# Kernel optimization log

Measured on AMD Instinct MI355X. Metric: run time of the kernel, lower is better.

## Reference

```python
import jax, jax.numpy as jnp
import numpy as np

ALPHA = 0.2          # LeakyReLU slope
THRESH = 0.6         # adjacency connection threshold
NEG_INF = -9e15      # masked-softmax fill used by the original


def setup_inputs() -> dict:
    key = jax.random.key(0)
    ks = jax.random.split(key, 5)
    B, N, F = 32, 512, 128
    h = jax.random.normal(ks[0], (B, N, F), dtype=jnp.float32)
    # torch nn.Linear weights: y = x @ W.T
    W = jax.random.normal(ks[1], (F, F), dtype=jnp.float32) * 0.1
    a = jax.random.normal(ks[2], (2 * F, 1), dtype=jnp.float32) * 0.1
    A0 = jax.random.normal(ks[3], (4 * N, N), dtype=jnp.float32) * 0.05
    A2 = jax.random.normal(ks[4], (N, 4 * N), dtype=jnp.float32) * 0.05
    return {"h": h, "W": W, "a": a, "A0": A0, "A2": A2}


def reference(h, W, a, A0, A2):
    F = W.shape[0]
    # Wh = W(h)                                  [B, N, F]
    Wh = jnp.einsum("bnf,gf->bng", h, W)
    # attention logits e = leakyrelu(Wh a1 + (Wh a2)^T)   [B, N, N]
    Wh1 = Wh @ a[:F]                              # [B, N, 1]
    Wh2 = Wh @ a[F:]                              # [B, N, 1]
    e = jax.nn.leaky_relu(Wh1 + jnp.swapaxes(Wh2, 1, 2), ALPHA)
    # learned adjacency MLP over last (node) dim: Linear -> Sigmoid -> Linear
    adj = e + jnp.einsum("bnk,mk->bnm", jax.nn.sigmoid(jnp.einsum("bnm,km->bnk", e, A0)), A2)
    # threshold + mask + softmax
    adj = jnp.where(adj > THRESH, adj, 0.0)
    att = jnp.where(adj > 0, e, NEG_INF)
    att = jax.nn.softmax(att, axis=2)
    # dropout is identity in eval mode
    h_prime = jnp.einsum("bnm,bmf->bnf", att, Wh)
    return jax.nn.elu(h_prime)                    # concat=True branch
```

## Files before the change

### kernel.cpp

```cpp
#include <hip/hip_runtime.h>

#define BB 32
#define NN 512
#define FF 128
#define K4 2048
#define ALPHA 0.2f
#define THRESH 0.6f
#define NEGINF -9e15f

typedef unsigned short u16;
typedef unsigned int u32;
typedef _Float16 f16;
typedef __attribute__((ext_vector_type(8))) _Float16 half8;
typedef __attribute__((ext_vector_type(4))) float f32x4;

union U16F { u16 u; f16 h; };
__device__ __forceinline__ u16 hbits(f16 h) { U16F x; x.h = h; return x.u; }
__device__ __forceinline__ float htof(u16 u) { U16F x; x.u = u; return (float)x.h; }
__device__ __forceinline__ void split2(float v, u16& hi, u16& lo) {
    f16 h = (f16)v;
    f16 l = (f16)(v - (float)h);
    hi = hbits(h);
    lo = hbits(l);
}
__device__ __forceinline__ float lrelu(float x) { return fmaxf(x, ALPHA * x); }

__device__ __forceinline__ void gload16(const void* g, void* l) {
    __builtin_amdgcn_global_load_lds(
        (__attribute__((address_space(1))) const unsigned int*)(unsigned long long)g,
        (__attribute__((address_space(3))) unsigned int*)(unsigned int)(unsigned long long)l,
        16, 0, 0);
}

__global__ void k_u(const float* __restrict__ W, const float* __restrict__ a,
                    float* __restrict__ u12) {
    int f = threadIdx.x;
    float s1 = 0.f, s2 = 0.f;
    for (int g = 0; g < FF; ++g) {
        float w = W[g * FF + f];
        s1 += w * a[g];
        s2 += w * a[FF + g];
    }
    u12[f] = s1;
    u12[FF + f] = s2;
}

__global__ void k_wh12(const float* __restrict__ h, const float* __restrict__ u12,
                       float* __restrict__ Wh12) {
    int row = blockIdx.x;
    int f = threadIdx.x;
    float hv = h[(size_t)row * FF + f];
    float p1 = hv * u12[f], p2 = hv * u12[FF + f];
#pragma unroll
    for (int o = 1; o < 64; o <<= 1) {
        p1 += __shfl_xor(p1, o, 64);
        p2 += __shfl_xor(p2, o, 64);
    }
    __shared__ float s1[2], s2[2];
    int w = f >> 6;
    if ((f & 63) == 0) { s1[w] = p1; s2[w] = p2; }
    __syncthreads();
    if (f == 0) {
        Wh12[row] = s1[0] + s1[1];
        Wh12[BB * NN + row] = s2[0] + s2[1];
    }
}

__global__ __launch_bounds__(256) void k_whT(const float* __restrict__ W,
                                             const float* __restrict__ h,
                                             u16* __restrict__ Thi, u16* __restrict__ Tlo) {
    const int bm = blockIdx.y * 64, bn = blockIdx.x * 64;
    __shared__ float As[32][68];
    __shared__ float Bs[32][68];
    int tid = threadIdx.x;
    int tx = tid & 15, ty = tid >> 4;
    float acc[4][4] = {{0.f}};
    int r = tid >> 3, q = tid & 7;
    const float* Ap = W + (size_t)(bm + r) * FF + q * 4;
    const float* Bp = h + (size_t)(bn + r) * FF + q * 4;
    for (int k0 = 0; k0 < FF; k0 += 32) {
        float4 a0 = *(const float4*)(Ap + k0);
        float4 a1 = *(const float4*)(Ap + k0 + 32 * FF);
        float4 b0 = *(const float4*)(Bp + k0);
        float4 b1 = *(const float4*)(Bp + k0 + 32 * FF);
        __syncthreads();
        As[q * 4 + 0][r] = a0.x; As[q * 4 + 1][r] = a0.y;
        As[q * 4 + 2][r] = a0.z; As[q * 4 + 3][r] = a0.w;
        As[q * 4 + 0][r + 32] = a1.x; As[q * 4 + 1][r + 32] = a1.y;
        As[q * 4 + 2][r + 32] = a1.z; As[q * 4 + 3][r + 32] = a1.w;
        Bs[q * 4 + 0][r] = b0.x; Bs[q * 4 + 1][r] = b0.y;
        Bs[q * 4 + 2][r] = b0.z; Bs[q * 4 + 3][r] = b0.w;
        Bs[q * 4 + 0][r + 32] = b1.x; Bs[q * 4 + 1][r + 32] = b1.y;
        Bs[q * 4 + 2][r + 32] = b1.z; Bs[q * 4 + 3][r + 32] = b1.w;
        __syncthreads();
#pragma unroll
        for (int kk = 0; kk < 32; ++kk) {
            float av[4], bv[4];
            *(float4*)av = *(const float4*)&As[kk][ty * 4];
            *(float4*)bv = *(const float4*)&Bs[kk][tx * 4];
#pragma unroll
            for (int i = 0; i < 4; ++i)
#pragma unroll
                for (int j = 0; j < 4; ++j) acc[i][j] = fmaf(av[i], bv[j], acc[i][j]);
        }
    }
#pragma unroll
    for (int i = 0; i < 4; ++i) {
        int f = bm + ty * 4 + i;
#pragma unroll
        for (int j = 0; j < 4; ++j) {
            int mg = bn + tx * 4 + j;
            u16 hi, lo;
            split2(acc[i][j], hi, lo);
            size_t idx = ((size_t)(mg >> 9) * FF + f) * NN + (mg & 511);
            Thi[idx] = hi;
            Tlo[idx] = lo;
        }
    }
}

__global__ void k_split(const float* __restrict__ X, u16* __restrict__ Hi,
                        u16* __restrict__ Lo, int n4) {
    int i = blockIdx.x * 256 + threadIdx.x;
    if (i >= n4) return;
    float4 v = *(const float4*)(X + (size_t)i * 4);
    ushort4 hh, ll;
    split2(v.x, hh.x, ll.x);
    split2(v.y, hh.y, ll.y);
    split2(v.z, hh.z, ll.z);
    split2(v.w, hh.w, ll.w);
    *(ushort4*)(Hi + (size_t)i * 4) = hh;
    *(ushort4*)(Lo + (size_t)i * 4) = ll;
}

__global__ __launch_bounds__(512) void k_g1(const float* __restrict__ Wh12, int c0,
                                            const u16* __restrict__ Bhi,
                                            const u16* __restrict__ Blo,
                                            u16* __restrict__ Shi, u16* __restrict__ Slo,
                                            int mblocks) {
    __shared__ __align__(16) u16 ldsA[8192];
    __shared__ __align__(16) u16 ldsB[16384];
    __shared__ float wh1s[128];
    __shared__ float wh2s[512];
    const int tid = threadIdx.x;
    const int l = tid & 63, w = tid >> 6;
    const int wm = w >> 2, wn = w & 3;
    const int nwg = gridDim.x, q = nwg >> 3;
    const int wg = (blockIdx.x & 7) * q + (blockIdx.x >> 3);
    const int nb = wg / mblocks, mb = wg % mblocks;
    const int bm = mb * 128, bn = nb * 256;
    const int bglob = c0 + (bm >> 9);

    if (tid < 128) wh1s[tid] = Wh12[(size_t)c0 * NN + bm + tid];
    if (tid < 512) wh2s[tid] = Wh12[BB * NN + (size_t)bglob * NN + tid];

    f32x4 acc[4][4];
#pragma unroll
    for (int m = 0; m < 4; ++m)
#pragma unroll
        for (int n = 0; n < 4; ++n) acc[m][n] = (f32x4){0.f, 0.f, 0.f, 0.f};

    const int gb0 = w * 2, gb1 = w * 2 + 1;
    const size_t rb0 = (size_t)(bn + gb0 * 16 + (l & 15)) * NN + ((l >> 4) * 8);
    const size_t rb1 = (size_t)(bn + gb1 * 16 + (l & 15)) * NN + ((l >> 4) * 8);
    const int arow = (tid >> 6) * 16 + (l & 15);
    const int akc = (l >> 4) * 8;

    __syncthreads();

    const float myw1 = wh1s[arow];

    for (int t = 0; t < 16; ++t) {
        const int k0 = t * 32;
        gload16(Bhi + rb0 + k0, &ldsB[gb0 * 512]);
        gload16(Bhi + rb1 + k0, &ldsB[gb1 * 512]);
        gload16(Blo + rb0 + k0, &ldsB[8192 + gb0 * 512]);
        gload16(Blo + rb1 + k0, &ldsB[8192 + gb1 * 512]);
        {
            const int kc = k0 + akc;
            float w2v[8];
            *(float4*)&w2v[0] = *(const float4*)&wh2s[kc];
            *(float4*)&w2v[4] = *(const float4*)&wh2s[kc + 4];
            u32 hh[4], llv[4];
#pragma unroll
            for (int jj = 0; jj < 4; ++jj) {
                float e0 = lrelu(myw1 + w2v[2 * jj]);
                float e1 = lrelu(myw1 + w2v[2 * jj + 1]);
                u16 h0, l0, h1, l1;
                split2(e0, h0, l0);
                split2(e1, h1, l1);
                hh[jj] = (u32)h0 | ((u32)h1 << 16);
                llv[jj] = (u32)l0 | ((u32)l1 << 16);
            }
            *(uint4*)&ldsA[tid * 8] = make_uint4(hh[0], hh[1], hh[2], hh[3]);
            *(uint4*)&ldsA[4096 + tid * 8] = make_uint4(llv[0], llv[1], llv[2], llv[3]);
        }
        __syncthreads();
        half8 bh[4], bl[4];
#pragma unroll
        for (int n = 0; n < 4; ++n) {
            const int gB = wn * 4 + n;
            bh[n] = *(const half8*)&ldsB[(gB * 64 + l) * 8];
            bl[n] = *(const half8*)&ldsB[8192 + (gB * 64 + l) * 8];
        }
#pragma unroll
        for (int m = 0; m < 4; ++m) {
            const int gA = wm * 4 + m;
            half8 ah = *(const half8*)&ldsA[(gA * 64 + l) * 8];
            half8 al = *(const half8*)&ldsA[4096 + (gA * 64 + l) * 8];
#pragma unroll
            for (int n = 0; n < 4; ++n)
                acc[m][n] = __builtin_amdgcn_mfma_f32_16x16x32_f16(ah, bh[n], acc[m][n], 0, 0, 0);
#pragma unroll
            for (int n = 0; n < 4; ++n)
                acc[m][n] = __builtin_amdgcn_mfma_f32_16x16x32_f16(al, bh[n], acc[m][n], 0, 0, 0);
#pragma unroll
            for (int n = 0; n < 4; ++n)
                acc[m][n] = __builtin_amdgcn_mfma_f32_16x16x32_f16(ah, bl[n], acc[m][n], 0, 0, 0);
        }
        __syncthreads();
    }

    const int lr = (l >> 4) * 4, lc = l & 15;
#pragma unroll
    for (int m = 0; m < 4; ++m) {
#pragma unroll
        for (int n = 0; n < 4; ++n) {
#pragma unroll
            for (int j = 0; j < 4; ++j) {
                const int row = bm + wm * 64 + m * 16 + lr + j;
                const int col = bn + wn * 64 + n * 16 + lc;
                const float s = 1.f / (1.f + __expf(-acc[m][n][j]));
                u16 hi, lo;
                split2(s, hi, lo);
                const size_t idx = (size_t)row * K4 + col;
                Shi[idx] = hi;
                Slo[idx] = lo;
            }
        }
    }
}

__global__ __launch_bounds__(256, 2) void k_g2(const u16* __restrict__ Ahi,
                                               const u16* __restrict__ Alo,
                                               const u16* __restrict__ Bhi,
                                               const u16* __restrict__ Blo,
                                               const float* __restrict__ Wh12, int c0,
                                               u32* __restrict__ ADJ) {
    __shared__ __align__(16) u16 ldsA[2][2][4096];
    __shared__ __align__(16) u16 ldsB[2][2][4096];
    const int tid = threadIdx.x;
    const int l = tid & 63, w = tid >> 6;
    const int wm = w >> 1, wn = w & 1;
    const int nwg = gridDim.x, q = nwg >> 3;
    const int wg = ((int)blockIdx.x & 7) * q + ((int)blockIdx.x >> 3);
    const int mb = wg >> 2, nb = wg & 3;
    const int bm = mb * 128, bn = nb * 128;

    const int ga0 = w * 2, ga1 = w * 2 + 1;
    const size_t ra0 = (size_t)(bm + ga0 * 16 + (l & 15)) * K4 + ((l >> 4) * 8);
    const size_t ra1 = (size_t)(bm + ga1 * 16 + (l & 15)) * K4 + ((l >> 4) * 8);
    const size_t rb0 = (size_t)(bn + ga0 * 16 + (l & 15)) * K4 + ((l >> 4) * 8);
    const size_t rb1 = (size_t)(bn + ga1 * 16 + (l & 15)) * K4 + ((l >> 4) * 8);

    auto STAGE = [&](int buf, int k0) {
        gload16(Ahi + ra0 + k0, &ldsA[buf][0][ga0 * 512]);
        gload16(Ahi + ra1 + k0, &ldsA[buf][0][ga1 * 512]);
        gload16(Alo + ra0 + k0, &ldsA[buf][1][ga0 * 512]);
        gload16(Alo + ra1 + k0, &ldsA[buf][1][ga1 * 512]);
        gload16(Bhi + rb0 + k0, &ldsB[buf][0][ga0 * 512]);
        gload16(Bhi + rb1 + k0, &ldsB[buf][0][ga1 * 512]);
        gload16(Blo + rb0 + k0, &ldsB[buf][1][ga0 * 512]);
        gload16(Blo + rb1 + k0, &ldsB[buf][1][ga1 * 512]);
    };

    f32x4 acc[4][4];
#pragma unroll
    for (int m = 0; m < 4; ++m)
#pragma unroll
        for (int n = 0; n < 4; ++n) acc[m][n] = (f32x4){0.f, 0.f, 0.f, 0.f};

    STAGE(0, 0);
    for (int t = 0; t < 64; ++t) {
        const int cur = t & 1;
        if (t < 63) {
            STAGE(cur ^ 1, (t + 1) * 32);
            asm volatile("s_waitcnt vmcnt(8)" ::: "memory");
        } else {
            asm volatile("s_waitcnt vmcnt(0)" ::: "memory");
        }
        __builtin_amdgcn_s_barrier();
        __builtin_amdgcn_sched_barrier(0);
        half8 bh[4], bl[4];
#pragma unroll
        for (int n = 0; n < 4; ++n) {
            const int gB = wn * 4 + n;
            bh[n] = *(const half8*)&ldsB[cur][0][(gB * 64 + l) * 8];
            bl[n] = *(const half8*)&ldsB[cur][1][(gB * 64 + l) * 8];
        }
        __builtin_amdgcn_s_setprio(1);
#pragma unroll
        for (int m = 0; m < 4; ++m) {
            const int gA = wm * 4 + m;
            half8 ah = *(const half8*)&ldsA[cur][0][(gA * 64 + l) * 8];
            half8 al = *(const half8*)&ldsA[cur][1][(gA * 64 + l) * 8];
#pragma unroll
            for (int n = 0; n < 4; ++n)
                acc[m][n] = __builtin_amdgcn_mfma_f32_16x16x32_f16(ah, bh[n], acc[m][n], 0, 0, 0);
#pragma unroll
            for (int n = 0; n < 4; ++n)
                acc[m][n] = __builtin_amdgcn_mfma_f32_16x16x32_f16(al, bh[n], acc[m][n], 0, 0, 0);
#pragma unroll
            for (int n = 0; n < 4; ++n)
                acc[m][n] = __builtin_amdgcn_mfma_f32_16x16x32_f16(ah, bl[n], acc[m][n], 0, 0, 0);
        }
        __builtin_amdgcn_s_setprio(0);
        __builtin_amdgcn_sched_barrier(0);
        __builtin_amdgcn_s_barrier();
    }

    const int bglob = c0 + (bm >> 9);
    const float* wh2p = Wh12 + BB * NN + (size_t)bglob * NN;
    const int lr = (l >> 4) * 4, lc = l & 15;
#pragma unroll
    for (int m = 0; m < 4; ++m) {
#pragma unroll
        for (int n = 0; n < 4; ++n) {
#pragma unroll
            for (int j = 0; j < 4; ++j) {
                const int row = bm + wm * 64 + m * 16 + lr + j;
                const int col = bn + wn * 64 + n * 16 + lc;
                const float e = lrelu(Wh12[(size_t)c0 * NN + row] + wh2p[col]);
                u32 pk = 0xFFFFFFFFu;
                if (e + acc[m][n][j] > THRESH) {
                    u16 hi, lo;
                    split2(e, hi, lo);
                    pk = (u32)hi | ((u32)lo << 16);
                }
                ADJ[(size_t)row * NN + col] = pk;
            }
        }
    }
}

__global__ __launch_bounds__(256) void k_softmax2(const u32* __restrict__ ADJ,
                                                  u16* __restrict__ Hi, u16* __restrict__ Lo) {
    const size_t row = blockIdx.x;
    const u32* p = ADJ + row * NN;
    const int t = threadIdx.x;
    u32 w0 = p[t], w1 = p[t + 256];
    float v0 = (w0 == 0xFFFFFFFFu) ? NEGINF : htof((u16)(w0 & 0xFFFF)) + htof((u16)(w0 >> 16));
    float v1 = (w1 == 0xFFFFFFFFu) ? NEGINF : htof((u16)(w1 & 0xFFFF)) + htof((u16)(w1 >> 16));
    float m = fmaxf(v0, v1);
#pragma unroll
    for (int o = 1; o < 64; o <<= 1) m = fmaxf(m, __shfl_xor(m, o, 64));
    __shared__ float red[4], red2[4];
    int w = t >> 6;
    if ((t & 63) == 0) red[w] = m;
    __syncthreads();
    m = fmaxf(fmaxf(red[0], red[1]), fmaxf(red[2], red[3]));
    float e0 = __expf(v0 - m), e1 = __expf(v1 - m);
    float s = e0 + e1;
#pragma unroll
    for (int o = 1; o < 64; o <<= 1) s += __shfl_xor(s, o, 64);
    if ((t & 63) == 0) red2[w] = s;
    __syncthreads();
    s = red2[0] + red2[1] + red2[2] + red2[3];
    float inv = 1.f / s;
    float a0 = e0 * inv, a1 = e1 * inv;
    u16 h0, l0, h1, l1;
    split2(a0, h0, l0);
    split2(a1, h1, l1);
    Hi[row * NN + t] = h0;
    Hi[row * NN + t + 256] = h1;
    Lo[row * NN + t] = l0;
    Lo[row * NN + t + 256] = l1;
}

__global__ __launch_bounds__(256) void k_pv(const u16* __restrict__ Ahi,
                                            const u16* __restrict__ Alo,
                                            const u16* __restrict__ Bhi,
                                            const u16* __restrict__ Blo,
                                            float* __restrict__ OUT) {
    __shared__ __align__(16) u16 lds[2][4][4096];
    const int tid = threadIdx.x;
    const int l = tid & 63, w = tid >> 6;
    const int wr = w >> 1, wc = w & 1;
    const int bz = blockIdx.z;
    const int bm = blockIdx.y * 128, bn = 0;

    const u16* A0p = Ahi + (size_t)bz * NN * NN;
    const u16* A1p = Alo + (size_t)bz * NN * NN;
    const u16* B0p = Bhi + (size_t)bz * FF * NN;
    const u16* B1p = Blo + (size_t)bz * FF * NN;

    const int g0 = w, g1 = w + 4;
    const size_t offA0 = (size_t)(bm + g0 * 16 + (l & 15)) * NN + (l >> 4) * 8;
    const size_t offA1 = (size_t)(bm + g1 * 16 + (l & 15)) * NN + (l >> 4) * 8;
    const size_t offB0 = (size_t)(bn + g0 * 16 + (l & 15)) * NN + (l >> 4) * 8;
    const size_t offB1 = (size_t)(bn + g1 * 16 + (l & 15)) * NN + (l >> 4) * 8;

    auto STAGE = [&](int buf, int kk) {
        gload16(A0p + offA0 + kk, &lds[buf][0][g0 * 512]);
        gload16(A0p + offA1 + kk, &lds[buf][0][g1 * 512]);
        gload16(A1p + offA0 + kk, &lds[buf][1][g0 * 512]);
        gload16(A1p + offA1 + kk, &lds[buf][1][g1 * 512]);
        gload16(B0p + offB0 + kk, &lds[buf][2][g0 * 512]);
        gload16(B0p + offB1 + kk, &lds[buf][2][g1 * 512]);
        gload16(B1p + offB0 + kk, &lds[buf][3][g0 * 512]);
        gload16(B1p + offB1 + kk, &lds[buf][3][g1 * 512]);
    };

    f32x4 acc[4][4];
#pragma unroll
    for (int m = 0; m < 4; ++m)
#pragma unroll
        for (int n = 0; n < 4; ++n) acc[m][n] = (f32x4){0.f, 0.f, 0.f, 0.f};

    STAGE(0, 0);
    for (int t = 0; t < 16; ++t) {
        const int cur = t & 1;
        if (t + 1 < 16) {
            STAGE(cur ^ 1, (t + 1) * 32);
            asm volatile("s_waitcnt vmcnt(8)" ::: "memory");
        } else {
            asm volatile("s_waitcnt vmcnt(0)" ::: "memory");
        }
        __builtin_amdgcn_s_barrier();
        __builtin_amdgcn_sched_barrier(0);
        half8 ah[4], al[4], bh[4], bl[4];
#pragma unroll
        for (int m = 0; m < 4; ++m) {
            ah[m] = *(const half8*)&lds[cur][0][((wr * 4 + m) * 64 + l) * 8];
            al[m] = *(const half8*)&lds[cur][1][((wr * 4 + m) * 64 + l) * 8];
        }
#pragma unroll
        for (int n = 0; n < 4; ++n) {
            bh[n] = *(const half8*)&lds[cur][2][((wc * 4 + n) * 64 + l) * 8];
            bl[n] = *(const half8*)&lds[cur][3][((wc * 4 + n) * 64 + l) * 8];
        }
#pragma unroll
        for (int m = 0; m < 4; ++m) {
#pragma unroll
            for (int n = 0; n < 4; ++n)
                acc[m][n] = __builtin_amdgcn_mfma_f32_16x16x32_f16(ah[m], bh[n], acc[m][n], 0, 0, 0);
        }
#pragma unroll
        for (int m = 0; m < 4; ++m) {
#pragma unroll
            for (int n = 0; n < 4; ++n) {
                acc[m][n] = __builtin_amdgcn_mfma_f32_16x16x32_f16(al[m], bh[n], acc[m][n], 0, 0, 0);
                acc[m][n] = __builtin_amdgcn_mfma_f32_16x16x32_f16(ah[m], bl[n], acc[m][n], 0, 0, 0);
            }
        }
        __builtin_amdgcn_s_barrier();
    }

    const int lr = (l >> 4) * 4, lc = l & 15;
#pragma unroll
    for (int m = 0; m < 4; ++m) {
#pragma unroll
        for (int n = 0; n < 4; ++n) {
#pragma unroll
            for (int j = 0; j < 4; ++j) {
                const int row = bm + wr * 64 + m * 16 + lr + j;
                const int col = bn + wc * 64 + n * 16 + lc;
                const float v = acc[m][n][j];
                OUT[(size_t)bz * NN * FF + (size_t)row * FF + col] =
                    v > 0.f ? v : __expf(v) - 1.f;
            }
        }
    }
}

extern "C" void kernel_launch(void* const* d_in, const int* in_sizes, int n_in,
                              void* d_out, int out_size, void* d_ws, size_t ws_size,
                              hipStream_t stream) {
    const float* h = (const float*)d_in[0];
    const float* W = (const float*)d_in[1];
    const float* a = (const float*)d_in[2];
    const float* A0 = (const float*)d_in[3];
    const float* A2 = (const float*)d_in[4];
    float* out = (float*)d_out;

    char* ws = (char*)d_ws;
    size_t ofs = 0;
    auto alloc = [&](size_t bytes) -> void* {
        void* p = ws + ofs;
        ofs = (ofs + bytes + 255) & ~(size_t)255;
        return p;
    };
    float* u12 = (float*)alloc(2 * FF * sizeof(float));
    float* Wh12 = (float*)alloc(2 * (size_t)BB * NN * sizeof(float));
    u16* WhThi = (u16*)alloc((size_t)BB * FF * NN * 2);
    u16* WhTlo = (u16*)alloc((size_t)BB * FF * NN * 2);
    u16* A0hi = (u16*)alloc((size_t)K4 * NN * 2);
    u16* A0lo = (u16*)alloc((size_t)K4 * NN * 2);
    u16* A2hi = (u16*)alloc((size_t)NN * K4 * 2);
    u16* A2lo = (u16*)alloc((size_t)NN * K4 * 2);

    const size_t per_b = (size_t)NN * K4 * 2 * 2 + (size_t)NN * NN * 4;
    int cb = BB;
    while (cb > 1 && ofs + (size_t)cb * per_b + 8192 > ws_size) cb >>= 1;
    u16* Shi = (u16*)alloc((size_t)cb * NN * K4 * 2);
    u16* Slo = (u16*)alloc((size_t)cb * NN * K4 * 2);
    u32* ADJ = (u32*)alloc((size_t)cb * NN * NN * 4);
    u16* AttHi = Shi;
    u16* AttLo = Slo;

    k_u<<<1, 128, 0, stream>>>(W, a, u12);
    k_wh12<<<BB * NN, 128, 0, stream>>>(h, u12, Wh12);
    k_whT<<<dim3((BB * NN) / 64, FF / 64), 256, 0, stream>>>(W, h, WhThi, WhTlo);
    k_split<<<(K4 * NN / 4 + 255) / 256, 256, 0, stream>>>(A0, A0hi, A0lo, K4 * NN / 4);
    k_split<<<(NN * K4 / 4 + 255) / 256, 256, 0, stream>>>(A2, A2hi, A2lo, NN * K4 / 4);

    for (int c0 = 0; c0 < BB; c0 += cb) {
        const int c = (BB - c0) < cb ? (BB - c0) : cb;
        const int mb1 = c * 4;
        k_g1<<<mb1 * (K4 / 256), 512, 0, stream>>>(Wh12, c0, A0hi, A0lo, Shi, Slo, mb1);
        k_g2<<<c * 16, 256, 0, stream>>>(Shi, Slo, A2hi, A2lo, Wh12, c0, ADJ);
        k_softmax2<<<c * NN, 256, 0, stream>>>(ADJ, AttHi, AttLo);
        k_pv<<<dim3(1, NN / 128, c), 256, 0, stream>>>(
            AttHi, AttLo, WhThi + (size_t)c0 * FF * NN, WhTlo + (size_t)c0 * FF * NN,
            out + (size_t)c0 * NN * FF);
    }
}
```

Baseline: 302.0 us.

## Split-K the second adjacency GEMM and move thresholding into softmax

```diff
diff --git a/kernel.cpp b/kernel.cpp
--- a/kernel.cpp
+++ b/kernel.cpp
@@ -241,38 +241,27 @@
     }
 }
 
-__global__ __launch_bounds__(256, 2) void k_g2(const u16* __restrict__ Ahi,
-                                               const u16* __restrict__ Alo,
-                                               const u16* __restrict__ Bhi,
-                                               const u16* __restrict__ Blo,
-                                               const float* __restrict__ Wh12, int c0,
-                                               u32* __restrict__ ADJ) {
-    __shared__ __align__(16) u16 ldsA[2][2][4096];
-    __shared__ __align__(16) u16 ldsB[2][2][4096];
+__global__ __launch_bounds__(256) void k_g2(const u16* __restrict__ Ahi,
+                                            const u16* __restrict__ Alo,
+                                            const u16* __restrict__ Bhi,
+                                            const u16* __restrict__ Blo,
+                                            float* __restrict__ PADJ, long sK) {
+    __shared__ __align__(16) u16 ldsA[8192];
+    __shared__ __align__(16) u16 ldsB[8192];
     const int tid = threadIdx.x;
     const int l = tid & 63, w = tid >> 6;
     const int wm = w >> 1, wn = w & 1;
     const int nwg = gridDim.x, q = nwg >> 3;
     const int wg = ((int)blockIdx.x & 7) * q + ((int)blockIdx.x >> 3);
-    const int mb = wg >> 2, nb = wg & 3;
+    const int nb = wg & 3, ks = (wg >> 2) & 1, mb = wg >> 3;
     const int bm = mb * 128, bn = nb * 128;
-
-    const int ga0 = w * 2, ga1 = w * 2 + 1;
-    const size_t ra0 = (size_t)(bm + ga0 * 16 + (l & 15)) * K4 + ((l >> 4) * 8);
-    const size_t ra1 = (size_t)(bm + ga1 * 16 + (l & 15)) * K4 + ((l >> 4) * 8);
-    const size_t rb0 = (size_t)(bn + ga0 * 16 + (l & 15)) * K4 + ((l >> 4) * 8);
-    const size_t rb1 = (size_t)(bn + ga1 * 16 + (l & 15)) * K4 + ((l >> 4) * 8);
-
-    auto STAGE = [&](int buf, int k0) {
-        gload16(Ahi + ra0 + k0, &ldsA[buf][0][ga0 * 512]);
-        gload16(Ahi + ra1 + k0, &ldsA[buf][0][ga1 * 512]);
-        gload16(Alo + ra0 + k0, &ldsA[buf][1][ga0 * 512]);
-        gload16(Alo + ra1 + k0, &ldsA[buf][1][ga1 * 512]);
-        gload16(Bhi + rb0 + k0, &ldsB[buf][0][ga0 * 512]);
-        gload16(Bhi + rb1 + k0, &ldsB[buf][0][ga1 * 512]);
-        gload16(Blo + rb0 + k0, &ldsB[buf][1][ga0 * 512]);
-        gload16(Blo + rb1 + k0, &ldsB[buf][1][ga1 * 512]);
-    };
+    const int kbase = ks * 1024;
+
+    const int g0 = w * 2, g1 = w * 2 + 1;
+    const size_t ra0 = (size_t)(bm + g0 * 16 + (l & 15)) * K4 + kbase + ((l >> 4) * 8);
+    const size_t ra1 = (size_t)(bm + g1 * 16 + (l & 15)) * K4 + kbase + ((l >> 4) * 8);
+    const size_t rb0 = (size_t)(bn + g0 * 16 + (l & 15)) * K4 + kbase + ((l >> 4) * 8);
+    const size_t rb1 = (size_t)(bn + g1 * 16 + (l & 15)) * K4 + kbase + ((l >> 4) * 8);
 
     f32x4 acc[4][4];
 #pragma unroll
@@ -280,30 +269,29 @@
 #pragma unroll
         for (int n = 0; n < 4; ++n) acc[m][n] = (f32x4){0.f, 0.f, 0.f, 0.f};
 
-    STAGE(0, 0);
-    for (int t = 0; t < 64; ++t) {
-        const int cur = t & 1;
-        if (t < 63) {
-            STAGE(cur ^ 1, (t + 1) * 32);
-            asm volatile("s_waitcnt vmcnt(8)" ::: "memory");
-        } else {
-            asm volatile("s_waitcnt vmcnt(0)" ::: "memory");
-        }
-        __builtin_amdgcn_s_barrier();
-        __builtin_amdgcn_sched_barrier(0);
+    for (int t = 0; t < 32; ++t) {
+        const int k0 = t * 32;
+        gload16(Ahi + ra0 + k0, &ldsA[g0 * 512]);
+        gload16(Ahi + ra1 + k0, &ldsA[g1 * 512]);
+        gload16(Alo + ra0 + k0, &ldsA[4096 + g0 * 512]);
+        gload16(Alo + ra1 + k0, &ldsA[4096 + g1 * 512]);
+        gload16(Bhi + rb0 + k0, &ldsB[g0 * 512]);
+        gload16(Bhi + rb1 + k0, &ldsB[g1 * 512]);
+        gload16(Blo + rb0 + k0, &ldsB[4096 + g0 * 512]);
+        gload16(Blo + rb1 + k0, &ldsB[4096 + g1 * 512]);
+        __syncthreads();
         half8 bh[4], bl[4];
 #pragma unroll
         for (int n = 0; n < 4; ++n) {
             const int gB = wn * 4 + n;
-            bh[n] = *(const half8*)&ldsB[cur][0][(gB * 64 + l) * 8];
-            bl[n] = *(const half8*)&ldsB[cur][1][(gB * 64 + l) * 8];
-        }
-        __builtin_amdgcn_s_setprio(1);
+            bh[n] = *(const half8*)&ldsB[(gB * 64 + l) * 8];
+            bl[n] = *(const half8*)&ldsB[4096 + (gB * 64 + l) * 8];
+        }
 #pragma unroll
         for (int m = 0; m < 4; ++m) {
             const int gA = wm * 4 + m;
-            half8 ah = *(const half8*)&ldsA[cur][0][(gA * 64 + l) * 8];
-            half8 al = *(const half8*)&ldsA[cur][1][(gA * 64 + l) * 8];
+            half8 ah = *(const half8*)&ldsA[(gA * 64 + l) * 8];
+            half8 al = *(const half8*)&ldsA[4096 + (gA * 64 + l) * 8];
 #pragma unroll
             for (int n = 0; n < 4; ++n)
                 acc[m][n] = __builtin_amdgcn_mfma_f32_16x16x32_f16(ah, bh[n], acc[m][n], 0, 0, 0);
@@ -314,13 +302,10 @@
             for (int n = 0; n < 4; ++n)
                 acc[m][n] = __builtin_amdgcn_mfma_f32_16x16x32_f16(ah, bl[n], acc[m][n], 0, 0, 0);
         }
-        __builtin_amdgcn_s_setprio(0);
-        __builtin_amdgcn_sched_barrier(0);
-        __builtin_amdgcn_s_barrier();
-    }
-
-    const int bglob = c0 + (bm >> 9);
-    const float* wh2p = Wh12 + BB * NN + (size_t)bglob * NN;
+        __syncthreads();
+    }
+
+    float* out = PADJ + (size_t)ks * sK;
     const int lr = (l >> 4) * 4, lc = l & 15;
 #pragma unroll
     for (int m = 0; m < 4; ++m) {
@@ -330,27 +315,30 @@
             for (int j = 0; j < 4; ++j) {
                 const int row = bm + wm * 64 + m * 16 + lr + j;
                 const int col = bn + wn * 64 + n * 16 + lc;
-                const float e = lrelu(Wh12[(size_t)c0 * NN + row] + wh2p[col]);
-                u32 pk = 0xFFFFFFFFu;
-                if (e + acc[m][n][j] > THRESH) {
-                    u16 hi, lo;
-                    split2(e, hi, lo);
-                    pk = (u32)hi | ((u32)lo << 16);
-                }
-                ADJ[(size_t)row * NN + col] = pk;
+                out[(size_t)row * NN + col] = acc[m][n][j];
             }
         }
     }
 }
 
-__global__ __launch_bounds__(256) void k_softmax2(const u32* __restrict__ ADJ,
+__global__ __launch_bounds__(256) void k_softmax2(const float* __restrict__ PADJ, long sK,
+                                                  const float* __restrict__ Wh12, int c0,
                                                   u16* __restrict__ Hi, u16* __restrict__ Lo) {
     const size_t row = blockIdx.x;
-    const u32* p = ADJ + row * NN;
     const int t = threadIdx.x;
-    u32 w0 = p[t], w1 = p[t + 256];
-    float v0 = (w0 == 0xFFFFFFFFu) ? NEGINF : htof((u16)(w0 & 0xFFFF)) + htof((u16)(w0 >> 16));
-    float v1 = (w1 == 0xFFFFFFFFu) ? NEGINF : htof((u16)(w1 & 0xFFFF)) + htof((u16)(w1 >> 16));
+    const float w1v = Wh12[(size_t)c0 * NN + row];
+    const int bglob = c0 + (int)(row >> 9);
+    const float* wh2p = Wh12 + BB * NN + (size_t)bglob * NN;
+    const float* p0 = PADJ + row * NN;
+    const float* p1 = PADJ + sK + row * NN;
+
+    float va = p0[t] + p1[t];
+    float vb = p0[t + 256] + p1[t + 256];
+    float ea = lrelu(w1v + wh2p[t]);
+    float eb = lrelu(w1v + wh2p[t + 256]);
+    float v0 = (ea + va > THRESH) ? ea : NEGINF;
+    float v1 = (eb + vb > THRESH) ? eb : NEGINF;
+
     float m = fmaxf(v0, v1);
 #pragma unroll
     for (int o = 1; o < 64; o <<= 1) m = fmaxf(m, __shfl_xor(m, o, 64));
@@ -499,12 +487,12 @@
     u16* A2hi = (u16*)alloc((size_t)NN * K4 * 2);
     u16* A2lo = (u16*)alloc((size_t)NN * K4 * 2);
 
-    const size_t per_b = (size_t)NN * K4 * 2 * 2 + (size_t)NN * NN * 4;
+    const size_t per_b = (size_t)NN * K4 * 2 * 2 + (size_t)NN * NN * 4 * 2;
     int cb = BB;
     while (cb > 1 && ofs + (size_t)cb * per_b + 8192 > ws_size) cb >>= 1;
     u16* Shi = (u16*)alloc((size_t)cb * NN * K4 * 2);
     u16* Slo = (u16*)alloc((size_t)cb * NN * K4 * 2);
-    u32* ADJ = (u32*)alloc((size_t)cb * NN * NN * 4);
+    float* PADJ = (float*)alloc((size_t)2 * cb * NN * NN * 4);
     u16* AttHi = Shi;
     u16* AttLo = Slo;
 
@@ -516,10 +504,11 @@
 
     for (int c0 = 0; c0 < BB; c0 += cb) {
         const int c = (BB - c0) < cb ? (BB - c0) : cb;
+        const long sK = (long)c * NN * NN;
         const int mb1 = c * 4;
         k_g1<<<mb1 * (K4 / 256), 512, 0, stream>>>(Wh12, c0, A0hi, A0lo, Shi, Slo, mb1);
-        k_g2<<<c * 16, 256, 0, stream>>>(Shi, Slo, A2hi, A2lo, Wh12, c0, ADJ);
-        k_softmax2<<<c * NN, 256, 0, stream>>>(ADJ, AttHi, AttLo);
+        k_g2<<<c * 32, 256, 0, stream>>>(Shi, Slo, A2hi, A2lo, PADJ, sK);
+        k_softmax2<<<c * NN, 256, 0, stream>>>(PADJ, sK, Wh12, c0, AttHi, AttLo);
         k_pv<<<dim3(1, NN / 128, c), 256, 0, stream>>>(
             AttHi, AttLo, WhThi + (size_t)c0 * FF * NN, WhTlo + (size_t)c0 * FF * NN,
             out + (size_t)c0 * NN * FF);
```

Result: slower. 316.4 us (+4.8%).
